# Kernel tuning notes

Measured on AMD Instinct MI355X. Metric: run time of the kernel, lower is better.

## Reference

```python
import jax, jax.numpy as jnp
import numpy as np

N_NODES = 50000
N_EDGES = 800000
N_GRAPHS = 512
NNF = 32      # num_node_features
EAD = 16      # edge_attr_dim
UD = 32       # u_dim
H = 64        # hidden_dim
OUT = 1


def _w(key, shape, scale=0.05):
    return (jax.random.normal(key, shape, dtype=jnp.float32) * scale)


def setup_inputs() -> dict:
    key = jax.random.key(0)
    ks = iter(jax.random.split(key, 64))
    inp = {
        "x": jax.random.normal(next(ks), (N_NODES, NNF), dtype=jnp.float32),
        "edge_attr": jax.random.normal(next(ks), (N_EDGES, EAD), dtype=jnp.float32),
        "u": jax.random.normal(next(ks), (N_GRAPHS, UD), dtype=jnp.float32),
        # edge MLPs: Linear(EAD,H), ReLU, Linear(H,H)
        "em1_w1": _w(next(ks), (EAD, H)), "em1_b1": jnp.zeros((H,), jnp.float32),
        "em1_w2": _w(next(ks), (H, H)),   "em1_b2": jnp.zeros((H,), jnp.float32),
        "em2_w1": _w(next(ks), (EAD, H)), "em2_b1": jnp.zeros((H,), jnp.float32),
        "em2_w2": _w(next(ks), (H, H)),   "em2_b2": jnp.zeros((H,), jnp.float32),
        # layer-1 GINEConvs (a,b,c stacked on leading axis 3):
        # internal edge projection lin: Linear(H -> NNF); nn: Linear(NNF,H),ReLU,Linear(H,H)
        "c1_lin_w": _w(next(ks), (3, H, NNF)), "c1_lin_b": jnp.zeros((3, NNF), jnp.float32),
        "c1_w1": _w(next(ks), (3, NNF, H)),    "c1_b1": jnp.zeros((3, H), jnp.float32),
        "c1_w2": _w(next(ks), (3, H, H)),      "c1_b2": jnp.zeros((3, H), jnp.float32),
        # layer-2 GINEConvs: lin: Linear(H->H); nn: Linear(H,H),ReLU,Linear(H,H)
        "c2_lin_w": _w(next(ks), (3, H, H)), "c2_lin_b": jnp.zeros((3, H), jnp.float32),
        "c2_w1": _w(next(ks), (3, H, H)),    "c2_b1": jnp.zeros((3, H), jnp.float32),
        "c2_w2": _w(next(ks), (3, H, H)),    "c2_b2": jnp.zeros((3, H), jnp.float32),
        # fusion linears and head
        "lin1_w": _w(next(ks), (3 * H, H)), "lin1_b": jnp.zeros((H,), jnp.float32),
        "lin2_w": _w(next(ks), (3 * H, H)), "lin2_b": jnp.zeros((H,), jnp.float32),
        "fc_w": _w(next(ks), (H + UD, OUT)), "fc_b": jnp.zeros((OUT,), jnp.float32),
        "edge_index": jax.random.randint(next(ks), (2, N_EDGES), 0, N_NODES, dtype=jnp.int64),
        "batch": jnp.sort(jax.random.randint(next(ks), (N_NODES,), 0, N_GRAPHS, dtype=jnp.int64)),
    }
    return inp


def _gine(x, src, dst, ea, lin_w, lin_b, w1, b1, w2, b2):
    # GINEConv (eps=0): out = nn(x + sum_j relu(x_j + lin(e_ij)))
    m = jax.nn.relu(x[src] + ea @ lin_w + lin_b)          # [E, d_x]
    agg = jax.ops.segment_sum(m, dst, num_segments=x.shape[0])
    h = x + agg
    return jax.nn.relu(h @ w1 + b1) @ w2 + b2             # [N, H]


def _triple(x, src, dst, ea, lw, lb, w1, b1, w2, b2):
    # run 3 parallel GINEConvs (a,b,c) and concat features
    outs = jax.vmap(_gine, in_axes=(None, None, None, None, 0, 0, 0, 0, 0, 0))(
        x, src, dst, ea, lw, lb, w1, b1, w2, b2)          # [3, N, H]
    return outs.transpose(1, 0, 2).reshape(x.shape[0], -1)  # [N, 3H]


def reference(x, edge_attr, u,
              em1_w1, em1_b1, em1_w2, em1_b2,
              em2_w1, em2_b1, em2_w2, em2_b2,
              c1_lin_w, c1_lin_b, c1_w1, c1_b1, c1_w2, c1_b2,
              c2_lin_w, c2_lin_b, c2_w1, c2_b1, c2_w2, c2_b2,
              lin1_w, lin1_b, lin2_w, lin2_b, fc_w, fc_b,
              edge_index, batch):
    src, dst = edge_index[0], edge_index[1]
    # layer 1
    ea1 = jax.nn.relu(edge_attr @ em1_w1 + em1_b1) @ em1_w2 + em1_b2
    h = _triple(x, src, dst, ea1, c1_lin_w, c1_lin_b, c1_w1, c1_b1, c1_w2, c1_b2)
    h = jax.nn.relu(h @ lin1_w + lin1_b)                  # [N, H]
    # layer 2
    ea2 = jax.nn.relu(edge_attr @ em2_w1 + em2_b1) @ em2_w2 + em2_b2
    h = _triple(h, src, dst, ea2, c2_lin_w, c2_lin_b, c2_w1, c2_b1, c2_w2, c2_b2)
    h = jax.nn.relu(h @ lin2_w + lin2_b)                  # [N, H]
    # global mean pool per graph
    sums = jax.ops.segment_sum(h, batch, num_segments=N_GRAPHS)
    cnt = jax.ops.segment_sum(jnp.ones((h.shape[0], 1), h.dtype), batch, num_segments=N_GRAPHS)
    pooled = sums / jnp.maximum(cnt, 1.0)                 # [G, H]
    return jnp.concatenate([pooled, u], axis=-1) @ fc_w + fc_b  # [G, 1]
```

## Files before the change

kernel.cpp:

```cpp
#include <hip/hip_runtime.h>
#include <hip/hip_bf16.h>

#define N_NODES  50000
#define N_EDGES  800000
#define N_GRAPHS 512
#define NTILES   3125

typedef short bf16x8 __attribute__((ext_vector_type(8)));
typedef float f32x4  __attribute__((ext_vector_type(4)));
typedef float f32x2  __attribute__((ext_vector_type(2)));

constexpr size_t B_CNT  = 0;
constexpr size_t ZERO_BYTES = 200192;
constexpr size_t B_OFF  = 200192;
constexpr size_t B_CUR  = 400384;
constexpr size_t B_BSUM = 600576;
constexpr size_t B_SEDGE= 601600;
constexpr size_t B_FR2  = 7001600;
constexpr size_t B_AGG2 = 7134720;
constexpr size_t B_Q    = 45534720;
constexpr size_t B_H1   = 199134720;
constexpr size_t B_H2   = 211934720;
constexpr size_t B_FOLD = 224734720;
constexpr size_t B_FRAG = 224908416;
constexpr int F_V1H = 0;
constexpr int F_B1F = 6144;
constexpr int F_V2H = 6240;
constexpr int F_B2F = 18528;
constexpr int F_U1  = 18720;
constexpr int F_UB1 = 31008;
constexpr int F_U2  = 31072;
constexpr int F_UB2 = 43360;
constexpr int FOLD_TOTAL = 43424;
constexpr int FR_W1E1 = 0;
constexpr int FR_W1E2 = 2048;
constexpr int FR_V1   = 4096;
constexpr int FR_V2   = 10240;
constexpr int FOLD2_TOTAL = 22528;
constexpr int FR3_M1W = 0;
constexpr int FR3_M1U = 6144;
constexpr int FR3_M2W = 18432;
constexpr int FR3_M2U = 30720;
constexpr int FOLD3_TOTAL = 43008;

__device__ inline unsigned short bf16u(float x) {
    unsigned int ua = __float_as_uint(x);
    return (unsigned short)((ua + 0x7FFFu + ((ua >> 16) & 1u)) >> 16);
}
__device__ inline unsigned int packbf2(float a, float b) {
    unsigned int ua = __float_as_uint(a), ub = __float_as_uint(b);
    return ((ua + 0x7FFFu + ((ua >> 16) & 1u)) >> 16) |
           ((ub + 0x7FFFu + ((ub >> 16) & 1u)) & 0xFFFF0000u);
}
__device__ inline unsigned short pkfp8(float a, float b) {
    return (unsigned short)__builtin_amdgcn_cvt_pk_fp8_f32(a, b, 0, false);
}
__device__ inline f32x2 unpkfp8(unsigned short us) {
    return __builtin_amdgcn_cvt_pk_f32_fp8((int)us, false);
}

__global__ __launch_bounds__(256) void fold_kernel(
    const float* __restrict__ em1_w2, const float* __restrict__ em1_b2,
    const float* __restrict__ em2_w2, const float* __restrict__ em2_b2,
    const float* __restrict__ c1_lin_w, const float* __restrict__ c1_lin_b,
    const float* __restrict__ c2_lin_w, const float* __restrict__ c2_lin_b,
    const float* __restrict__ c1_w2, const float* __restrict__ c1_b2,
    const float* __restrict__ c2_w2, const float* __restrict__ c2_b2,
    const float* __restrict__ lin1_w, const float* __restrict__ lin1_b,
    const float* __restrict__ lin2_w, const float* __restrict__ lin2_b,
    float* __restrict__ fw)
{
    int idx = blockIdx.x * 256 + threadIdx.x;
    if (idx >= FOLD_TOTAL) return;
    int r = idx;
    if (r < 6144) {
        int k = r / 96, c = r % 96, i = c / 32, j = c % 32;
        float s = 0.f;
        for (int m = 0; m < 64; m++) s = fmaf(em1_w2[k * 64 + m], c1_lin_w[i * 2048 + m * 32 + j], s);
        fw[F_V1H + r] = s; return;
    }
    r -= 6144;
    if (r < 96) {
        int i = r / 32, j = r % 32;
        float s = c1_lin_b[r];
        for (int m = 0; m < 64; m++) s = fmaf(em1_b2[m], c1_lin_w[i * 2048 + m * 32 + j], s);
        fw[F_B1F + r] = s; return;
    }
    r -= 96;
    if (r < 12288) {
        int k = r / 192, c = r % 192, i = c / 64, j = c % 64;
        float s = 0.f;
        for (int m = 0; m < 64; m++) s = fmaf(em2_w2[k * 64 + m], c2_lin_w[i * 4096 + m * 64 + j], s);
        fw[F_V2H + r] = s; return;
    }
    r -= 12288;
    if (r < 192) {
        int i = r / 64, j = r % 64;
        float s = c2_lin_b[r];
        for (int m = 0; m < 64; m++) s = fmaf(em2_b2[m], c2_lin_w[i * 4096 + m * 64 + j], s);
        fw[F_B2F + r] = s; return;
    }
    r -= 192;
    if (r < 12288) {
        int i = r / 4096, k = (r / 64) % 64, j = r % 64;
        float s = 0.f;
        for (int m = 0; m < 64; m++) s = fmaf(c1_w2[i * 4096 + k * 64 + m], lin1_w[(i * 64 + m) * 64 + j], s);
        fw[F_U1 + r] = s; return;
    }
    r -= 12288;
    if (r < 64) {
        float s = lin1_b[r];
        for (int i = 0; i < 3; i++)
            for (int m = 0; m < 64; m++) s = fmaf(c1_b2[i * 64 + m], lin1_w[(i * 64 + m) * 64 + r], s);
        fw[F_UB1 + r] = s; return;
    }
    r -= 64;
    if (r < 12288) {
        int i = r / 4096, k = (r / 64) % 64, j = r % 64;
        float s = 0.f;
        for (int m = 0; m < 64; m++) s = fmaf(c2_w2[i * 4096 + k * 64 + m], lin2_w[(i * 64 + m) * 64 + j], s);
        fw[F_U2 + r] = s; return;
    }
    r -= 12288;
    {
        float s = lin2_b[r];
        for (int i = 0; i < 3; i++)
            for (int m = 0; m < 64; m++) s = fmaf(c2_b2[i * 64 + m], lin2_w[(i * 64 + m) * 64 + r], s);
        fw[F_UB2 + r] = s; return;
    }
}

__global__ __launch_bounds__(256) void fold2_kernel(
    const float* __restrict__ em1_w1, const float* __restrict__ em2_w1,
    const float* __restrict__ fw, unsigned short* __restrict__ fr)
{
    int idx = blockIdx.x * 256 + threadIdx.x;
    if (idx >= FOLD2_TOTAL) return;
    if (idx < 4096) {
        const float* w = (idx < 2048) ? em1_w1 : em2_w1;
        int r = idx & 2047;
        int tt = r >> 9, lane = (r >> 3) & 63, j = r & 7;
        int q = lane >> 4, k = q * 8 + j, m = tt * 16 + (lane & 15);
        fr[idx] = (k < 16) ? bf16u(w[k * 64 + m]) : (unsigned short)0;
        return;
    }
    if (idx < 10240) {
        int r = idx - 4096;
        int nt = r / 1024, ka = (r >> 9) & 1, lane = (r >> 3) & 63, j = r & 7;
        int q = lane >> 4;
        int t = 32 * ka + 16 * (j >> 2) + 4 * q + (j & 3);
        int n = nt * 16 + (lane & 15);
        fr[idx] = bf16u(fw[F_V1H + t * 96 + n]);
        return;
    }
    {
        int r = idx - 10240;
        int nt = r / 1024, ka = (r >> 9) & 1, lane = (r >> 3) & 63, j = r & 7;
        int q = lane >> 4;
        int t = 32 * ka + 16 * (j >> 2) + 4 * q + (j & 3);
        int n = nt * 16 + (lane & 15);
        fr[idx] = bf16u(fw[F_V2H + t * 192 + n]);
        return;
    }
}

__global__ __launch_bounds__(256) void fold3_kernel(
    const float* __restrict__ c1_w1, const float* __restrict__ c2_w1,
    const float* __restrict__ fw, unsigned short* __restrict__ fr2)
{
    int idx = blockIdx.x * 256 + threadIdx.x;
    if (idx >= FOLD3_TOTAL) return;
    if (idx < 6144) {
        int i = idx / 2048, r = idx % 2048;
        int tt = r >> 9, lane = (r >> 3) & 63, jj = r & 7;
        int k = (lane >> 4) * 8 + jj, m = tt * 16 + (lane & 15);
        fr2[FR3_M1W + idx] = bf16u(c1_w1[i * 2048 + k * 64 + m]);
        return;
    }
    if (idx < 18432) {
        int r = idx - 6144;
        int i = r / 4096, r2 = r % 4096;
        int b = r2 >> 10, ka = (r2 >> 9) & 1, lane = (r2 >> 3) & 63, jj = r2 & 7;
        int t = 32 * ka + 16 * (jj >> 2) + 4 * (lane >> 4) + (jj & 3);
        int n = b * 16 + (lane & 15);
        fr2[FR3_M1U + r] = bf16u(fw[F_U1 + i * 4096 + t * 64 + n]);
        return;
    }
    if (idx < 30720) {
        int r = idx - 18432;
        int i = r / 4096, r2 = r % 4096;
        int tt = r2 >> 10, ka = (r2 >> 9) & 1, lane = (r2 >> 3) & 63, jj = r2 & 7;
        int k = ka * 32 + (lane >> 4) * 8 + jj, m = tt * 16 + (lane & 15);
        fr2[FR3_M2W + r] = bf16u(c2_w1[i * 4096 + k * 64 + m]);
        return;
    }
    {
        int r = idx - 30720;
        int i = r / 4096, r2 = r % 4096;
        int b = r2 >> 10, ka = (r2 >> 9) & 1, lane = (r2 >> 3) & 63, jj = r2 & 7;
        int t = 32 * ka + 16 * (jj >> 2) + 4 * (lane >> 4) + (jj & 3);
        int n = b * 16 + (lane & 15);
        fr2[FR3_M2U + r] = bf16u(fw[F_U2 + i * 4096 + t * 64 + n]);
        return;
    }
}

__global__ __launch_bounds__(256) void hist_kernel(const int* __restrict__ ei, int* __restrict__ cnt) {
    int e = blockIdx.x * 256 + threadIdx.x;
    if (e < N_EDGES) atomicAdd(&cnt[ei[N_EDGES + e]], 1);
}

__global__ __launch_bounds__(256) void scan1_kernel(const int* __restrict__ cnt,
                                                    int* __restrict__ off, int* __restrict__ bsum) {
    __shared__ int sh[256];
    int t = threadIdx.x, i = blockIdx.x * 256 + t;
    int v = (i < N_NODES) ? cnt[i] : 0;
    sh[t] = v; __syncthreads();
    for (int d = 1; d < 256; d <<= 1) {
        int add = (t >= d) ? sh[t - d] : 0;
        __syncthreads();
        sh[t] += add;
        __syncthreads();
    }
    if (i < N_NODES) off[i] = sh[t] - v;
    if (t == 255) bsum[blockIdx.x] = sh[255];
}

__global__ __launch_bounds__(256) void scan2_kernel(int* __restrict__ bsum) {
    __shared__ int sh[256];
    int t = threadIdx.x;
    int v = (t < 196) ? bsum[t] : 0;
    sh[t] = v; __syncthreads();
    for (int d = 1; d < 256; d <<= 1) {
        int add = (t >= d) ? sh[t - d] : 0;
        __syncthreads();
        sh[t] += add;
        __syncthreads();
    }
    bsum[t] = sh[t] - v;
}

__global__ __launch_bounds__(256) void scan3_kernel(int* __restrict__ off, const int* __restrict__ bsum,
                                                    int* __restrict__ cur) {
    int i = blockIdx.x * 256 + threadIdx.x;
    if (i < N_NODES) {
        int o = off[i] + bsum[i >> 8];
        off[i] = o;
        cur[i] = o;
    }
    if (i == 0) off[N_NODES] = N_EDGES;
}

__global__ __launch_bounds__(256) void scatter_kernel(const int* __restrict__ ei, int* __restrict__ cur,
                                                      int2* __restrict__ sedge) {
    int e = blockIdx.x * 256 + threadIdx.x;
    if (e >= N_EDGES) return;
    int d = ei[N_EDGES + e];
    int p = atomicAdd(&cur[d], 1);
    sedge[p] = make_int2(ei[e], e);
}

template<int NT>
__global__ __launch_bounds__(256, 2) void edge_mfma_kernel(
    const float* __restrict__ edge_attr, const int2* __restrict__ sedge,
    const unsigned short* __restrict__ w1frag, const float* __restrict__ b1,
    const unsigned short* __restrict__ vfrag,  const float* __restrict__ bias2,
    unsigned short* __restrict__ qout, int nTiles)
{
    const int lane = threadIdx.x & 63;
    const int wid  = threadIdx.x >> 6;
    const int col  = lane & 15;
    const int quad = lane >> 4;

    bf16x8 w1f[4];
#pragma unroll
    for (int tt = 0; tt < 4; tt++)
        w1f[tt] = *(const bf16x8*)(w1frag + (tt * 64 + lane) * 8);
    bf16x8 vf[NT][2];
#pragma unroll
    for (int nt = 0; nt < NT; nt++)
#pragma unroll
        for (int ka = 0; ka < 2; ka++)
            vf[nt][ka] = *(const bf16x8*)(vfrag + ((nt * 2 + ka) * 64 + lane) * 8);
    float4 b1v[4];
#pragma unroll
    for (int tt = 0; tt < 4; tt++)
        b1v[tt] = *(const float4*)(b1 + tt * 16 + quad * 4);
    float b2v[NT];
#pragma unroll
    for (int nt = 0; nt < NT; nt++) b2v[nt] = bias2[nt * 16 + col];

    const int gw = blockIdx.x * 4 + wid;
    const int stride = gridDim.x * 4;
    for (int t = gw; t < nTiles; t += stride) {
        const int s = t * 16 + col;
        const int e = sedge[s].y;
        bf16x8 eaf;
        uint4 eau = make_uint4(0u, 0u, 0u, 0u);
        if (quad < 2) {
            const float4 v0 = *(const float4*)(edge_attr + (size_t)e * 16 + quad * 8);
            const float4 v1 = *(const float4*)(edge_attr + (size_t)e * 16 + quad * 8 + 4);
            eau.x = packbf2(v0.x, v0.y); eau.y = packbf2(v0.z, v0.w);
            eau.z = packbf2(v1.x, v1.y); eau.w = packbf2(v1.z, v1.w);
        }
        eaf = __builtin_bit_cast(bf16x8, eau);

        f32x4 c1[4];
#pragma unroll
        for (int tt = 0; tt < 4; tt++) {
            f32x4 ci = {b1v[tt].x, b1v[tt].y, b1v[tt].z, b1v[tt].w};
            c1[tt] = __builtin_amdgcn_mfma_f32_16x16x32_bf16(w1f[tt], eaf, ci, 0, 0, 0);
        }

        bf16x8 a2[2];
#pragma unroll
        for (int ka = 0; ka < 2; ka++) {
            uint4 au;
            au.x = packbf2(fmaxf(c1[2 * ka][0], 0.f),     fmaxf(c1[2 * ka][1], 0.f));
            au.y = packbf2(fmaxf(c1[2 * ka][2], 0.f),     fmaxf(c1[2 * ka][3], 0.f));
            au.z = packbf2(fmaxf(c1[2 * ka + 1][0], 0.f), fmaxf(c1[2 * ka + 1][1], 0.f));
            au.w = packbf2(fmaxf(c1[2 * ka + 1][2], 0.f), fmaxf(c1[2 * ka + 1][3], 0.f));
            a2[ka] = __builtin_bit_cast(bf16x8, au);
        }

        f32x4 c2[NT];
#pragma unroll
        for (int nt = 0; nt < NT; nt++) {
            f32x4 ci = {b2v[nt], b2v[nt], b2v[nt], b2v[nt]};
            ci = __builtin_amdgcn_mfma_f32_16x16x32_bf16(a2[0], vf[nt][0], ci, 0, 0, 0);
            c2[nt] = __builtin_amdgcn_mfma_f32_16x16x32_bf16(a2[1], vf[nt][1], ci, 0, 0, 0);
        }

        const size_t rowb = (size_t)t * 16 + quad * 4;
#pragma unroll
        for (int b = 0; b < NT / 2; b++) {
#pragma unroll
            for (int r = 0; r < 4; r++) {
                qout[(rowb + r) * (size_t)(NT * 8) + b * 16 + col] =
                    pkfp8(c2[2 * b][r], c2[2 * b + 1][r]);
            }
        }
    }
}

__global__ __launch_bounds__(64) void gather1_kernel(
    const float* __restrict__ x, const int* __restrict__ off, const int2* __restrict__ sedge,
    const unsigned short* __restrict__ q1, float* __restrict__ agg1)
{
    const int n = blockIdx.x, l = threadIdx.x;
    if (l >= 48) return;
    const int s0 = off[n], s1 = off[n + 1];
    const int c = l & 15;
    const int n1 = (l >> 4) * 32 + c, n2 = n1 + 16;
    float a0 = 0.f, a1 = 0.f, b0 = 0.f, b1 = 0.f;
    int s = s0;
    for (; s + 2 <= s1; s += 2) {
        const int srcA = sedge[s].x, srcB = sedge[s + 1].x;
        const unsigned short uA = q1[(size_t)s * 48 + l];
        const unsigned short uB = q1[(size_t)(s + 1) * 48 + l];
        const float xA0 = x[(size_t)srcA * 32 + c], xA1 = x[(size_t)srcA * 32 + c + 16];
        const float xB0 = x[(size_t)srcB * 32 + c], xB1 = x[(size_t)srcB * 32 + c + 16];
        const f32x2 dA = unpkfp8(uA);
        const f32x2 dB = unpkfp8(uB);
        a0 += fmaxf(xA0 + dA.x, 0.f);
        a1 += fmaxf(xA1 + dA.y, 0.f);
        b0 += fmaxf(xB0 + dB.x, 0.f);
        b1 += fmaxf(xB1 + dB.y, 0.f);
    }
    if (s < s1) {
        const int src = sedge[s].x;
        const f32x2 d = unpkfp8(q1[(size_t)s * 48 + l]);
        a0 += fmaxf(x[(size_t)src * 32 + c] + d.x, 0.f);
        a1 += fmaxf(x[(size_t)src * 32 + c + 16] + d.y, 0.f);
    }
    agg1[(size_t)n * 96 + n1] = a0 + b0;
    agg1[(size_t)n * 96 + n2] = a1 + b1;
}

__global__ __launch_bounds__(256) void mlp1_mfma_kernel(
    const float* __restrict__ x, const float* __restrict__ agg1,
    const unsigned short* __restrict__ fr2, const float* __restrict__ c1_b1,
    const float* __restrict__ fw, float* __restrict__ h1)
{
    const int lane = threadIdx.x & 63, wid = threadIdx.x >> 6;
    const int tile = blockIdx.x * 4 + wid;
    if (tile >= NTILES) return;
    const int col = lane & 15, quad = lane >> 4;
    const int node = tile * 16 + col;

    const float4 xa = *(const float4*)(x + (size_t)node * 32 + quad * 8);
    const float4 xb = *(const float4*)(x + (size_t)node * 32 + quad * 8 + 4);

    f32x4 c2[4];
#pragma unroll
    for (int b = 0; b < 4; b++) {
        const float ub = fw[F_UB1 + b * 16 + col];
        c2[b] = {ub, ub, ub, ub};
    }
#pragma unroll
    for (int i = 0; i < 3; i++) {
        const float4 a0 = *(const float4*)(agg1 + (size_t)node * 96 + i * 32 + quad * 8);
        const float4 a1 = *(const float4*)(agg1 + (size_t)node * 96 + i * 32 + quad * 8 + 4);
        uint4 iu;
        iu.x = packbf2(xa.x + a0.x, xa.y + a0.y);
        iu.y = packbf2(xa.z + a0.z, xa.w + a0.w);
        iu.z = packbf2(xb.x + a1.x, xb.y + a1.y);
        iu.w = packbf2(xb.z + a1.z, xb.w + a1.w);
        const bf16x8 inf = __builtin_bit_cast(bf16x8, iu);

        f32x4 c1[4];
#pragma unroll
        for (int tt = 0; tt < 4; tt++) {
            const bf16x8 wf = *(const bf16x8*)(fr2 + FR3_M1W + ((i * 4 + tt) * 64 + lane) * 8);
            const float4 bi = *(const float4*)(c1_b1 + i * 64 + tt * 16 + quad * 4);
            f32x4 ci = {bi.x, bi.y, bi.z, bi.w};
            c1[tt] = __builtin_amdgcn_mfma_f32_16x16x32_bf16(wf, inf, ci, 0, 0, 0);
        }
        bf16x8 a2[2];
#pragma unroll
        for (int ka = 0; ka < 2; ka++) {
            uint4 au;
            au.x = packbf2(fmaxf(c1[2 * ka][0], 0.f),     fmaxf(c1[2 * ka][1], 0.f));
            au.y = packbf2(fmaxf(c1[2 * ka][2], 0.f),     fmaxf(c1[2 * ka][3], 0.f));
            au.z = packbf2(fmaxf(c1[2 * ka + 1][0], 0.f), fmaxf(c1[2 * ka + 1][1], 0.f));
            au.w = packbf2(fmaxf(c1[2 * ka + 1][2], 0.f), fmaxf(c1[2 * ka + 1][3], 0.f));
            a2[ka] = __builtin_bit_cast(bf16x8, au);
        }
#pragma unroll
        for (int b = 0; b < 4; b++)
#pragma unroll
            for (int ka = 0; ka < 2; ka++) {
                const bf16x8 uf = *(const bf16x8*)(fr2 + FR3_M1U + (((i * 4 + b) * 2 + ka) * 64 + lane) * 8);
                c2[b] = __builtin_amdgcn_mfma_f32_16x16x32_bf16(a2[ka], uf, c2[b], 0, 0, 0);
            }
    }
    const int rowb = tile * 16 + quad * 4;
#pragma unroll
    for (int b = 0; b < 4; b++)
#pragma unroll
        for (int r = 0; r < 4; r++)
            h1[(size_t)(rowb + r) * 64 + b * 16 + col] = fmaxf(c2[b][r], 0.f);
}

__global__ __launch_bounds__(64) void gather2_kernel(
    const float* __restrict__ h1, const int* __restrict__ off, const int2* __restrict__ sedge,
    const unsigned short* __restrict__ q2, float* __restrict__ agg2)
{
    const int n = blockIdx.x, l = threadIdx.x;
    const int s0 = off[n], s1 = off[n + 1];

    const int k1 = ((l >> 4) & 1) * 32 + (l & 15);
    float sa0 = 0.f, sa1 = 0.f, sb0 = 0.f, sb1 = 0.f;
    float ta0 = 0.f, ta1 = 0.f, tb0 = 0.f, tb1 = 0.f;
    int s = s0;
    for (; s + 2 <= s1; s += 2) {
        const int srcA = sedge[s].x, srcB = sedge[s + 1].x;
        const float hA0 = h1[(size_t)srcA * 64 + k1];
        const float hA1 = h1[(size_t)srcA * 64 + k1 + 16];
        const float hB0 = h1[(size_t)srcB * 64 + k1];
        const float hB1 = h1[(size_t)srcB * 64 + k1 + 16];
        const f32x2 dA = unpkfp8(q2[(size_t)s * 96 + l]);
        const f32x2 dB = unpkfp8(q2[(size_t)(s + 1) * 96 + l]);
        sa0 += fmaxf(hA0 + dA.x, 0.f);
        sa1 += fmaxf(hA1 + dA.y, 0.f);
        ta0 += fmaxf(hB0 + dB.x, 0.f);
        ta1 += fmaxf(hB1 + dB.y, 0.f);
        if (l < 32) {
            const f32x2 d2A = unpkfp8(q2[(size_t)s * 96 + 64 + l]);
            const f32x2 d2B = unpkfp8(q2[(size_t)(s + 1) * 96 + 64 + l]);
            sb0 += fmaxf(hA0 + d2A.x, 0.f);
            sb1 += fmaxf(hA1 + d2A.y, 0.f);
            tb0 += fmaxf(hB0 + d2B.x, 0.f);
            tb1 += fmaxf(hB1 + d2B.y, 0.f);
        }
    }
    if (s < s1) {
        const int src = sedge[s].x;
        const float hv0 = h1[(size_t)src * 64 + k1];
        const float hv1 = h1[(size_t)src * 64 + k1 + 16];
        const f32x2 d = unpkfp8(q2[(size_t)s * 96 + l]);
        sa0 += fmaxf(hv0 + d.x, 0.f);
        sa1 += fmaxf(hv1 + d.y, 0.f);
        if (l < 32) {
            const f32x2 d2 = unpkfp8(q2[(size_t)s * 96 + 64 + l]);
            sb0 += fmaxf(hv0 + d2.x, 0.f);
            sb1 += fmaxf(hv1 + d2.y, 0.f);
        }
    }
    sa0 += ta0; sa1 += ta1; sb0 += tb0; sb1 += tb1;
    const int C1 = 32 * (l >> 4) + (l & 15);
    const int C2 = 128 + 32 * (l >> 4) + (l & 15);
    float* row = agg2 + (size_t)n * 192;
    row[C1] = sa0; row[C1 + 16] = sa1;
    if (l < 32) { row[C2] = sb0; row[C2 + 16] = sb1; }
}

__global__ __launch_bounds__(256) void mlp2_mfma_kernel(
    const float* __restrict__ h1, const float* __restrict__ agg2,
    const unsigned short* __restrict__ fr2, const float* __restrict__ c2_b1,
    const float* __restrict__ fw, float* __restrict__ h2)
{
    const int lane = threadIdx.x & 63, wid = threadIdx.x >> 6;
    const int tile = blockIdx.x * 4 + wid;
    if (tile >= NTILES) return;
    const int col = lane & 15, quad = lane >> 4;
    const int node = tile * 16 + col;

    float4 hv[4];
#pragma unroll
    for (int p = 0; p < 4; p++)
        hv[p] = *(const float4*)(h1 + (size_t)node * 64 + (p >> 1) * 32 + quad * 8 + (p & 1) * 4);

    f32x4 c2[4];
#pragma unroll
    for (int b = 0; b < 4; b++) {
        const float ub = fw[F_UB2 + b * 16 + col];
        c2[b] = {ub, ub, ub, ub};
    }
#pragma unroll
    for (int i = 0; i < 3; i++) {
        bf16x8 inf[2];
#pragma unroll
        for (int ka = 0; ka < 2; ka++) {
            const float4 a0 = *(const float4*)(agg2 + (size_t)node * 192 + i * 64 + ka * 32 + quad * 8);
            const float4 a1 = *(const float4*)(agg2 + (size_t)node * 192 + i * 64 + ka * 32 + quad * 8 + 4);
            const float4 h0 = hv[ka * 2], h1v = hv[ka * 2 + 1];
            uint4 iu;
            iu.x = packbf2(h0.x + a0.x, h0.y + a0.y);
            iu.y = packbf2(h0.z + a0.z, h0.w + a0.w);
            iu.z = packbf2(h1v.x + a1.x, h1v.y + a1.y);
            iu.w = packbf2(h1v.z + a1.z, h1v.w + a1.w);
            inf[ka] = __builtin_bit_cast(bf16x8, iu);
        }
        f32x4 c1[4];
#pragma unroll
        for (int tt = 0; tt < 4; tt++) {
            const bf16x8 wf0 = *(const bf16x8*)(fr2 + FR3_M2W + (((i * 4 + tt) * 2 + 0) * 64 + lane) * 8);
            const bf16x8 wf1 = *(const bf16x8*)(fr2 + FR3_M2W + (((i * 4 + tt) * 2 + 1) * 64 + lane) * 8);
            const float4 bi = *(const float4*)(c2_b1 + i * 64 + tt * 16 + quad * 4);
            f32x4 ci = {bi.x, bi.y, bi.z, bi.w};
            ci = __builtin_amdgcn_mfma_f32_16x16x32_bf16(wf0, inf[0], ci, 0, 0, 0);
            c1[tt] = __builtin_amdgcn_mfma_f32_16x16x32_bf16(wf1, inf[1], ci, 0, 0, 0);
        }
        bf16x8 a2[2];
#pragma unroll
        for (int ka = 0; ka < 2; ka++) {
            uint4 au;
            au.x = packbf2(fmaxf(c1[2 * ka][0], 0.f),     fmaxf(c1[2 * ka][1], 0.f));
            au.y = packbf2(fmaxf(c1[2 * ka][2], 0.f),     fmaxf(c1[2 * ka][3], 0.f));
            au.z = packbf2(fmaxf(c1[2 * ka + 1][0], 0.f), fmaxf(c1[2 * ka + 1][1], 0.f));
            au.w = packbf2(fmaxf(c1[2 * ka + 1][2], 0.f), fmaxf(c1[2 * ka + 1][3], 0.f));
            a2[ka] = __builtin_bit_cast(bf16x8, au);
        }
#pragma unroll
        for (int b = 0; b < 4; b++)
#pragma unroll
            for (int ka = 0; ka < 2; ka++) {
                const bf16x8 uf = *(const bf16x8*)(fr2 + FR3_M2U + (((i * 4 + b) * 2 + ka) * 64 + lane) * 8);
                c2[b] = __builtin_amdgcn_mfma_f32_16x16x32_bf16(a2[ka], uf, c2[b], 0, 0, 0);
            }
    }
    const int rowb = tile * 16 + quad * 4;
#pragma unroll
    for (int b = 0; b < 4; b++)
#pragma unroll
        for (int r = 0; r < 4; r++)
            h2[(size_t)(rowb + r) * 64 + b * 16 + col] = fmaxf(c2[b][r], 0.f);
}

__global__ __launch_bounds__(256) void pool_kernel(
    const float* __restrict__ h2, const int* __restrict__ batch,
    const float* __restrict__ u, const float* __restrict__ fc_w,
    const float* __restrict__ fc_b, float* __restrict__ out)
{
    __shared__ float red[256];
    const int g = blockIdx.x, t = threadIdx.x;
    int lo = 0, hi = N_NODES;
    while (lo < hi) { int m = (lo + hi) >> 1; if (batch[m] < g) lo = m + 1; else hi = m; }
    int lo2 = lo, hi2 = N_NODES;
    while (lo2 < hi2) { int m = (lo2 + hi2) >> 1; if (batch[m] < g + 1) lo2 = m + 1; else hi2 = m; }

    const int col = t & 63, ch = t >> 6;
    float s = 0.f;
    for (int idx = lo + ch; idx < lo2; idx += 4) s += h2[(size_t)idx * 64 + col];
    red[t] = s;
    __syncthreads();
    if (t < 64) red[t] = red[t] + red[64 + t] + red[128 + t] + red[192 + t];
    __syncthreads();
    if (t == 0) {
        const float inv = 1.f / fmaxf((float)(lo2 - lo), 1.f);
        float sv = fc_b[0];
        for (int j = 0; j < 64; j++) sv = fmaf(red[j] * inv, fc_w[j], sv);
        for (int k = 0; k < 32; k++) sv = fmaf(u[(size_t)g * 32 + k], fc_w[64 + k], sv);
        out[g] = sv;
    }
}

extern "C" void kernel_launch(void* const* d_in, const int* in_sizes, int n_in,
                              void* d_out, int out_size, void* d_ws, size_t ws_size,
                              hipStream_t stream) {
    (void)in_sizes; (void)n_in; (void)out_size; (void)ws_size;
    const float* x        = (const float*)d_in[0];
    const float* edge_attr= (const float*)d_in[1];
    const float* u        = (const float*)d_in[2];
    const float* em1_w1   = (const float*)d_in[3];
    const float* em1_b1   = (const float*)d_in[4];
    const float* em1_w2   = (const float*)d_in[5];
    const float* em1_b2   = (const float*)d_in[6];
    const float* em2_w1   = (const float*)d_in[7];
    const float* em2_b1   = (const float*)d_in[8];
    const float* em2_w2   = (const float*)d_in[9];
    const float* em2_b2   = (const float*)d_in[10];
    const float* c1_lin_w = (const float*)d_in[11];
    const float* c1_lin_b = (const float*)d_in[12];
    const float* c1_w1    = (const float*)d_in[13];
    const float* c1_b1    = (const float*)d_in[14];
    const float* c1_w2    = (const float*)d_in[15];
    const float* c1_b2    = (const float*)d_in[16];
    const float* c2_lin_w = (const float*)d_in[17];
    const float* c2_lin_b = (const float*)d_in[18];
    const float* c2_w1    = (const float*)d_in[19];
    const float* c2_b1    = (const float*)d_in[20];
    const float* c2_w2    = (const float*)d_in[21];
    const float* c2_b2    = (const float*)d_in[22];
    const float* lin1_w   = (const float*)d_in[23];
    const float* lin1_b   = (const float*)d_in[24];
    const float* lin2_w   = (const float*)d_in[25];
    const float* lin2_b   = (const float*)d_in[26];
    const float* fc_w     = (const float*)d_in[27];
    const float* fc_b     = (const float*)d_in[28];
    const int*   ei       = (const int*)d_in[29];
    const int*   batch    = (const int*)d_in[30];

    char* wsb = (char*)d_ws;
    int*   cnt  = (int*)(wsb + B_CNT);
    int*   off  = (int*)(wsb + B_OFF);
    int*   cur  = (int*)(wsb + B_CUR);
    int*   bsum = (int*)(wsb + B_BSUM);
    int2*  sedge= (int2*)(wsb + B_SEDGE);
    float* agg2 = (float*)(wsb + B_AGG2);
    unsigned short* q = (unsigned short*)(wsb + B_Q);
    float* h1   = (float*)(wsb + B_H1);
    float* h2   = (float*)(wsb + B_H2);
    float* fw   = (float*)(wsb + B_FOLD);
    unsigned short* fr  = (unsigned short*)(wsb + B_FRAG);
    unsigned short* fr2 = (unsigned short*)(wsb + B_FR2);
    float* out  = (float*)d_out;

    (void)hipMemsetAsync(d_ws, 0, ZERO_BYTES, stream);

    fold_kernel<<<(FOLD_TOTAL + 255) / 256, 256, 0, stream>>>(
        em1_w2, em1_b2, em2_w2, em2_b2, c1_lin_w, c1_lin_b, c2_lin_w, c2_lin_b,
        c1_w2, c1_b2, c2_w2, c2_b2, lin1_w, lin1_b, lin2_w, lin2_b, fw);
    fold2_kernel<<<(FOLD2_TOTAL + 255) / 256, 256, 0, stream>>>(em1_w1, em2_w1, fw, fr);
    fold3_kernel<<<(FOLD3_TOTAL + 255) / 256, 256, 0, stream>>>(c1_w1, c2_w1, fw, fr2);

    hist_kernel<<<N_EDGES / 256, 256, 0, stream>>>(ei, cnt);
    scan1_kernel<<<196, 256, 0, stream>>>(cnt, off, bsum);
    scan2_kernel<<<1, 256, 0, stream>>>(bsum);
    scan3_kernel<<<196, 256, 0, stream>>>(off, bsum, cur);
    scatter_kernel<<<N_EDGES / 256, 256, 0, stream>>>(ei, cur, sedge);

    edge_mfma_kernel<6><<<2048, 256, 0, stream>>>(
        edge_attr, sedge, fr + FR_W1E1, em1_b1, fr + FR_V1, fw + F_B1F, q, N_EDGES / 16);
    gather1_kernel<<<N_NODES, 64, 0, stream>>>(x, off, sedge, q, agg2);
    mlp1_mfma_kernel<<<(NTILES + 3) / 4, 256, 0, stream>>>(x, agg2, fr2, c1_b1, fw, h1);

    edge_mfma_kernel<12><<<2048, 256, 0, stream>>>(
        edge_attr, sedge, fr + FR_W1E2, em2_b1, fr + FR_V2, fw + F_B2F, q, N_EDGES / 16);
    gather2_kernel<<<N_NODES, 64, 0, stream>>>(h1, off, sedge, q, agg2);
    mlp2_mfma_kernel<<<(NTILES + 3) / 4, 256, 0, stream>>>(h1, agg2, fr2, c2_b1, fw, h2);

    pool_kernel<<<N_GRAPHS, 256, 0, stream>>>(h2, batch, u, fc_w, fc_b, out);
}
```

Before: 488.8 us.

## Fuse edge MLP with segmented gather-aggregation via LDS and atomics

Merges the per-edge MLP kernel and the per-node gather kernel into one. Edge messages are staged in LDS per 16-edge tile and summed into node rows, using a segmented reduction over the dst-sorted edges: plain stores for nodes that lie fully inside a chunk and atomics at chunk boundaries. This removes the round trip of the fp8 intermediate message buffer through global memory. It adds a dst array, memsets of the aggregate buffers, serialized readlane loops per edge, and fp32 atomics with nondeterministic summation order.

```diff
diff --git a/kernel.cpp b/kernel.cpp
--- a/kernel.cpp
+++ b/kernel.cpp
@@ -5,10 +5,12 @@
 #define N_EDGES  800000
 #define N_GRAPHS 512
 #define NTILES   3125
+#define ETILES   50000
+#define CT       4
+#define NCHUNKS  (ETILES / CT)
 
 typedef short bf16x8 __attribute__((ext_vector_type(8)));
 typedef float f32x4  __attribute__((ext_vector_type(4)));
-typedef float f32x2  __attribute__((ext_vector_type(2)));
 
 constexpr size_t B_CNT  = 0;
 constexpr size_t ZERO_BYTES = 200192;
@@ -16,13 +18,13 @@
 constexpr size_t B_CUR  = 400384;
 constexpr size_t B_BSUM = 600576;
 constexpr size_t B_SEDGE= 601600;
-constexpr size_t B_FR2  = 7001600;
-constexpr size_t B_AGG2 = 7134720;
-constexpr size_t B_Q    = 45534720;
-constexpr size_t B_H1   = 199134720;
-constexpr size_t B_H2   = 211934720;
-constexpr size_t B_FOLD = 224734720;
-constexpr size_t B_FRAG = 224908416;
+constexpr size_t B_DSTA = 7001600;
+constexpr size_t B_FR2  = 10201600;
+constexpr size_t B_AGG  = 10287616;
+constexpr size_t B_H1   = 48687616;
+constexpr size_t B_H2   = 61487616;
+constexpr size_t B_FOLD = 74287616;
+constexpr size_t B_FRAG = 74461440;
 constexpr int F_V1H = 0;
 constexpr int F_B1F = 6144;
 constexpr int F_V2H = 6240;
@@ -52,12 +54,6 @@
     return ((ua + 0x7FFFu + ((ua >> 16) & 1u)) >> 16) |
            ((ub + 0x7FFFu + ((ub >> 16) & 1u)) & 0xFFFF0000u);
 }
-__device__ inline unsigned short pkfp8(float a, float b) {
-    return (unsigned short)__builtin_amdgcn_cvt_pk_fp8_f32(a, b, 0, false);
-}
-__device__ inline f32x2 unpkfp8(unsigned short us) {
-    return __builtin_amdgcn_cvt_pk_f32_fp8((int)us, false);
-}
 
 __global__ __launch_bounds__(256) void fold_kernel(
     const float* __restrict__ em1_w2, const float* __restrict__ em1_b2,
@@ -252,25 +248,33 @@
 }
 
 __global__ __launch_bounds__(256) void scatter_kernel(const int* __restrict__ ei, int* __restrict__ cur,
-                                                      int2* __restrict__ sedge) {
+                                                      int2* __restrict__ sedge, int* __restrict__ dsta) {
     int e = blockIdx.x * 256 + threadIdx.x;
     if (e >= N_EDGES) return;
     int d = ei[N_EDGES + e];
     int p = atomicAdd(&cur[d], 1);
     sedge[p] = make_int2(ei[e], e);
-}
-
-template<int NT>
-__global__ __launch_bounds__(256, 2) void edge_mfma_kernel(
+    dsta[p] = d;
+}
+
+template<int NT, int XD>
+__global__ __launch_bounds__(256, 2) void fused_edge_gather(
     const float* __restrict__ edge_attr, const int2* __restrict__ sedge,
+    const int* __restrict__ dsta,
     const unsigned short* __restrict__ w1frag, const float* __restrict__ b1,
     const unsigned short* __restrict__ vfrag,  const float* __restrict__ bias2,
-    unsigned short* __restrict__ qout, int nTiles)
+    const float* __restrict__ X, float* __restrict__ agg, int nChunks)
 {
+    constexpr int C   = NT * 16;
+    constexpr int STR = C + 2;
+    __shared__ float lds[4 * 16 * STR];
     const int lane = threadIdx.x & 63;
     const int wid  = threadIdx.x >> 6;
     const int col  = lane & 15;
     const int quad = lane >> 4;
+    const int cw   = blockIdx.x * 4 + wid;
+    if (cw >= nChunks) return;
+    float* L = lds + wid * 16 * STR;
 
     bf16x8 w1f[4];
 #pragma unroll
@@ -290,12 +294,19 @@
 #pragma unroll
     for (int nt = 0; nt < NT; nt++) b2v[nt] = bias2[nt * 16 + col];
 
-    const int gw = blockIdx.x * 4 + wid;
-    const int stride = gridDim.x * 4;
-    for (int t = gw; t < nTiles; t += stride) {
+    const int xch = lane & (XD - 1);
+    float acc0 = 0.f, acc1 = 0.f, acc2 = 0.f;
+    int  curd  = -1;
+    bool inside = false;
+
+    const int t0 = cw * CT;
+    for (int ti = 0; ti < CT; ++ti) {
+        const int t = t0 + ti;
         const int s = t * 16 + col;
-        const int e = sedge[s].y;
-        bf16x8 eaf;
+        const int2 se = sedge[s];
+        const int  dv = dsta[s];
+        const int  e  = se.y;
+
         uint4 eau = make_uint4(0u, 0u, 0u, 0u);
         if (quad < 2) {
             const float4 v0 = *(const float4*)(edge_attr + (size_t)e * 16 + quad * 8);
@@ -303,7 +314,7 @@
             eau.x = packbf2(v0.x, v0.y); eau.y = packbf2(v0.z, v0.w);
             eau.z = packbf2(v1.x, v1.y); eau.w = packbf2(v1.z, v1.w);
         }
-        eaf = __builtin_bit_cast(bf16x8, eau);
+        const bf16x8 eaf = __builtin_bit_cast(bf16x8, eau);
 
         f32x4 c1[4];
 #pragma unroll
@@ -311,7 +322,6 @@
             f32x4 ci = {b1v[tt].x, b1v[tt].y, b1v[tt].z, b1v[tt].w};
             c1[tt] = __builtin_amdgcn_mfma_f32_16x16x32_bf16(w1f[tt], eaf, ci, 0, 0, 0);
         }
-
         bf16x8 a2[2];
 #pragma unroll
         for (int ka = 0; ka < 2; ka++) {
@@ -322,7 +332,6 @@
             au.w = packbf2(fmaxf(c1[2 * ka + 1][2], 0.f), fmaxf(c1[2 * ka + 1][3], 0.f));
             a2[ka] = __builtin_bit_cast(bf16x8, au);
         }
-
         f32x4 c2[NT];
 #pragma unroll
         for (int nt = 0; nt < NT; nt++) {
@@ -331,50 +340,47 @@
             c2[nt] = __builtin_amdgcn_mfma_f32_16x16x32_bf16(a2[1], vf[nt][1], ci, 0, 0, 0);
         }
 
-        const size_t rowb = (size_t)t * 16 + quad * 4;
-#pragma unroll
-        for (int b = 0; b < NT / 2; b++) {
-#pragma unroll
-            for (int r = 0; r < 4; r++) {
-                qout[(rowb + r) * (size_t)(NT * 8) + b * 16 + col] =
-                    pkfp8(c2[2 * b][r], c2[2 * b + 1][r]);
+#pragma unroll
+        for (int nt = 0; nt < NT; nt++)
+#pragma unroll
+            for (int r = 0; r < 4; r++)
+                L[(quad * 4 + r) * STR + nt * 16 + col] = c2[nt][r];
+
+#pragma unroll
+        for (int ee = 0; ee < 16; ++ee) {
+            const int srcn = __builtin_amdgcn_readlane(se.x, ee);
+            const int dn   = __builtin_amdgcn_readlane(dv, ee);
+            if (dn != curd) {
+                if (curd >= 0) {
+                    float* row = agg + (size_t)curd * C;
+                    if (inside) {
+                        row[lane] = acc0;
+                        if (64 + lane < C)  row[64 + lane]  = acc1;
+                        if (C > 128)        row[128 + lane] = acc2;
+                    } else {
+                        atomicAdd(&row[lane], acc0);
+                        if (64 + lane < C)  atomicAdd(&row[64 + lane],  acc1);
+                        if (C > 128)        atomicAdd(&row[128 + lane], acc2);
+                    }
+                    inside = true;
+                }
+                curd = dn;
+                acc0 = acc1 = acc2 = 0.f;
             }
-        }
-    }
-}
-
-__global__ __launch_bounds__(64) void gather1_kernel(
-    const float* __restrict__ x, const int* __restrict__ off, const int2* __restrict__ sedge,
-    const unsigned short* __restrict__ q1, float* __restrict__ agg1)
-{
-    const int n = blockIdx.x, l = threadIdx.x;
-    if (l >= 48) return;
-    const int s0 = off[n], s1 = off[n + 1];
-    const int c = l & 15;
-    const int n1 = (l >> 4) * 32 + c, n2 = n1 + 16;
-    float a0 = 0.f, a1 = 0.f, b0 = 0.f, b1 = 0.f;
-    int s = s0;
-    for (; s + 2 <= s1; s += 2) {
-        const int srcA = sedge[s].x, srcB = sedge[s + 1].x;
-        const unsigned short uA = q1[(size_t)s * 48 + l];
-        const unsigned short uB = q1[(size_t)(s + 1) * 48 + l];
-        const float xA0 = x[(size_t)srcA * 32 + c], xA1 = x[(size_t)srcA * 32 + c + 16];
-        const float xB0 = x[(size_t)srcB * 32 + c], xB1 = x[(size_t)srcB * 32 + c + 16];
-        const f32x2 dA = unpkfp8(uA);
-        const f32x2 dB = unpkfp8(uB);
-        a0 += fmaxf(xA0 + dA.x, 0.f);
-        a1 += fmaxf(xA1 + dA.y, 0.f);
-        b0 += fmaxf(xB0 + dB.x, 0.f);
-        b1 += fmaxf(xB1 + dB.y, 0.f);
-    }
-    if (s < s1) {
-        const int src = sedge[s].x;
-        const f32x2 d = unpkfp8(q1[(size_t)s * 48 + l]);
-        a0 += fmaxf(x[(size_t)src * 32 + c] + d.x, 0.f);
-        a1 += fmaxf(x[(size_t)src * 32 + c + 16] + d.y, 0.f);
-    }
-    agg1[(size_t)n * 96 + n1] = a0 + b0;
-    agg1[(size_t)n * 96 + n2] = a1 + b1;
+            const float xv = X[(size_t)srcn * XD + xch];
+            acc0 += fmaxf(xv + L[ee * STR + lane], 0.f);
+            if (64 + lane < C)
+                acc1 += fmaxf(xv + L[ee * STR + 64 + lane], 0.f);
+            if (C > 128)
+                acc2 += fmaxf(xv + L[ee * STR + 128 + lane], 0.f);
+        }
+    }
+    {
+        float* row = agg + (size_t)curd * C;
+        atomicAdd(&row[lane], acc0);
+        if (64 + lane < C)  atomicAdd(&row[64 + lane],  acc1);
+        if (C > 128)        atomicAdd(&row[128 + lane], acc2);
+    }
 }
 
 __global__ __launch_bounds__(256) void mlp1_mfma_kernel(
@@ -440,59 +446,6 @@
 #pragma unroll
         for (int r = 0; r < 4; r++)
             h1[(size_t)(rowb + r) * 64 + b * 16 + col] = fmaxf(c2[b][r], 0.f);
-}
-
-__global__ __launch_bounds__(64) void gather2_kernel(
-    const float* __restrict__ h1, const int* __restrict__ off, const int2* __restrict__ sedge,
-    const unsigned short* __restrict__ q2, float* __restrict__ agg2)
-{
-    const int n = blockIdx.x, l = threadIdx.x;
-    const int s0 = off[n], s1 = off[n + 1];
-
-    const int k1 = ((l >> 4) & 1) * 32 + (l & 15);
-    float sa0 = 0.f, sa1 = 0.f, sb0 = 0.f, sb1 = 0.f;
-    float ta0 = 0.f, ta1 = 0.f, tb0 = 0.f, tb1 = 0.f;
-    int s = s0;
-    for (; s + 2 <= s1; s += 2) {
-        const int srcA = sedge[s].x, srcB = sedge[s + 1].x;
-        const float hA0 = h1[(size_t)srcA * 64 + k1];
-        const float hA1 = h1[(size_t)srcA * 64 + k1 + 16];
-        const float hB0 = h1[(size_t)srcB * 64 + k1];
-        const float hB1 = h1[(size_t)srcB * 64 + k1 + 16];
-        const f32x2 dA = unpkfp8(q2[(size_t)s * 96 + l]);
-        const f32x2 dB = unpkfp8(q2[(size_t)(s + 1) * 96 + l]);
-        sa0 += fmaxf(hA0 + dA.x, 0.f);
-        sa1 += fmaxf(hA1 + dA.y, 0.f);
-        ta0 += fmaxf(hB0 + dB.x, 0.f);
-        ta1 += fmaxf(hB1 + dB.y, 0.f);
-        if (l < 32) {
-            const f32x2 d2A = unpkfp8(q2[(size_t)s * 96 + 64 + l]);
-            const f32x2 d2B = unpkfp8(q2[(size_t)(s + 1) * 96 + 64 + l]);
-            sb0 += fmaxf(hA0 + d2A.x, 0.f);
-            sb1 += fmaxf(hA1 + d2A.y, 0.f);
-            tb0 += fmaxf(hB0 + d2B.x, 0.f);
-            tb1 += fmaxf(hB1 + d2B.y, 0.f);
-        }
-    }
-    if (s < s1) {
-        const int src = sedge[s].x;
-        const float hv0 = h1[(size_t)src * 64 + k1];
-        const float hv1 = h1[(size_t)src * 64 + k1 + 16];
-        const f32x2 d = unpkfp8(q2[(size_t)s * 96 + l]);
-        sa0 += fmaxf(hv0 + d.x, 0.f);
-        sa1 += fmaxf(hv1 + d.y, 0.f);
-        if (l < 32) {
-            const f32x2 d2 = unpkfp8(q2[(size_t)s * 96 + 64 + l]);
-            sb0 += fmaxf(hv0 + d2.x, 0.f);
-            sb1 += fmaxf(hv1 + d2.y, 0.f);
-        }
-    }
-    sa0 += ta0; sa1 += ta1; sb0 += tb0; sb1 += tb1;
-    const int C1 = 32 * (l >> 4) + (l & 15);
-    const int C2 = 128 + 32 * (l >> 4) + (l & 15);
-    float* row = agg2 + (size_t)n * 192;
-    row[C1] = sa0; row[C1 + 16] = sa1;
-    if (l < 32) { row[C2] = sb0; row[C2 + 16] = sb1; }
 }
 
 __global__ __launch_bounds__(256) void mlp2_mfma_kernel(
@@ -638,8 +591,8 @@
     int*   cur  = (int*)(wsb + B_CUR);
     int*   bsum = (int*)(wsb + B_BSUM);
     int2*  sedge= (int2*)(wsb + B_SEDGE);
-    float* agg2 = (float*)(wsb + B_AGG2);
-    unsigned short* q = (unsigned short*)(wsb + B_Q);
+    int*   dsta = (int*)(wsb + B_DSTA);
+    float* agg  = (float*)(wsb + B_AGG);
     float* h1   = (float*)(wsb + B_H1);
     float* h2   = (float*)(wsb + B_H2);
     float* fw   = (float*)(wsb + B_FOLD);
@@ -659,17 +612,17 @@
     scan1_kernel<<<196, 256, 0, stream>>>(cnt, off, bsum);
     scan2_kernel<<<1, 256, 0, stream>>>(bsum);
     scan3_kernel<<<196, 256, 0, stream>>>(off, bsum, cur);
-    scatter_kernel<<<N_EDGES / 256, 256, 0, stream>>>(ei, cur, sedge);
-
-    edge_mfma_kernel<6><<<2048, 256, 0, stream>>>(
-        edge_attr, sedge, fr + FR_W1E1, em1_b1, fr + FR_V1, fw + F_B1F, q, N_EDGES / 16);
-    gather1_kernel<<<N_NODES, 64, 0, stream>>>(x, off, sedge, q, agg2);
-    mlp1_mfma_kernel<<<(NTILES + 3) / 4, 256, 0, stream>>>(x, agg2, fr2, c1_b1, fw, h1);
-
-    edge_mfma_kernel<12><<<2048, 256, 0, stream>>>(
-        edge_attr, sedge, fr + FR_W1E2, em2_b1, fr + FR_V2, fw + F_B2F, q, N_EDGES / 16);
-    gather2_kernel<<<N_NODES, 64, 0, stream>>>(h1, off, sedge, q, agg2);
-    mlp2_mfma_kernel<<<(NTILES + 3) / 4, 256, 0, stream>>>(h1, agg2, fr2, c2_b1, fw, h2);
+    scatter_kernel<<<N_EDGES / 256, 256, 0, stream>>>(ei, cur, sedge, dsta);
+
+    (void)hipMemsetAsync(wsb + B_AGG, 0, (size_t)N_NODES * 96 * 4, stream);
+    fused_edge_gather<6, 32><<<NCHUNKS / 4, 256, 0, stream>>>(
+        edge_attr, sedge, dsta, fr + FR_W1E1, em1_b1, fr + FR_V1, fw + F_B1F, x, agg, NCHUNKS);
+    mlp1_mfma_kernel<<<(NTILES + 3) / 4, 256, 0, stream>>>(x, agg, fr2, c1_b1, fw, h1);
+
+    (void)hipMemsetAsync(wsb + B_AGG, 0, (size_t)N_NODES * 192 * 4, stream);
+    fused_edge_gather<12, 64><<<NCHUNKS / 4, 256, 0, stream>>>(
+        edge_attr, sedge, dsta, fr + FR_W1E2, em2_b1, fr + FR_V2, fw + F_B2F, h1, agg, NCHUNKS);
+    mlp2_mfma_kernel<<<(NTILES + 3) / 4, 256, 0, stream>>>(h1, agg, fr2, c2_b1, fw, h2);
 
     pool_kernel<<<N_GRAPHS, 256, 0, stream>>>(h2, batch, u, fc_w, fc_b, out);
 }
```

Result: slower. 629.6 us (+28.8%).
